# Kernel optimization log

Hardware: AMD Instinct MI355X
Metric: run time of the kernel (lower is better)

## Reference

```python
import jax, jax.numpy as jnp
import numpy as np

B, T, D = 2, 2048, 1024
H, DH = 16, 64          # num_heads, size_per_head
NU = H * DH             # num_units == 1024


def setup_inputs() -> dict:
    key = jax.random.key(0)
    ks = jax.random.split(key, 8)
    s = 0.02
    return {
        "queries": jax.random.normal(ks[0], (B, T, D), jnp.float32),
        "keys": jax.random.normal(ks[1], (B, T, D), jnp.float32),
        "Wq": jax.random.normal(ks[2], (D, NU), jnp.float32) * s,
        "bq": jnp.zeros((NU,), jnp.float32),
        "Wk": jax.random.normal(ks[3], (D, NU), jnp.float32) * s,
        "bk": jnp.zeros((NU,), jnp.float32),
        "Wv": jax.random.normal(ks[4], (D, NU), jnp.float32) * s,
        "bv": jnp.zeros((NU,), jnp.float32),
    }


def reference(queries, keys, Wq, bq, Wk, bk, Wv, bv):
    # QKV projections
    q = queries @ Wq + bq            # [B, T, NU]
    k = keys @ Wk + bk
    v = keys @ Wv + bv
    # split heads: [B, T, H, DH] -> [B, H, T, DH]
    q_ = q.reshape(B, T, H, DH).transpose(0, 2, 1, 3)
    k_ = k.reshape(B, T, H, DH).transpose(0, 2, 1, 3)
    v_ = v.reshape(B, T, H, DH).transpose(0, 2, 1, 3)
    # scores scaled by num_units**-0.5 (full hidden dim, as in source)
    scores = jnp.einsum("bhqd,bhkd->bhqk", q_, k_) * (NU ** -0.5)
    # causal mask: triu(ones).T == lower-triangular; zeros -> -inf
    causal = jnp.tril(jnp.ones((T, T), bool))
    scores = jnp.where(causal, scores, -jnp.inf)
    weights = jax.nn.softmax(scores, axis=-1)   # [B, H, T, T]
    # dropout is identity in eval/reference
    out = jnp.einsum("bhqk,bhkd->bhqd", weights, v_)  # [B, H, T, DH]
    # merge heads back to [B, T, NU]
    out = out.transpose(0, 2, 1, 3).reshape(B, T, NU)
    return out, weights
```

## Files before the change

kernel.cpp:

```cpp
#include <hip/hip_runtime.h>
#include <cstddef>
#include <cstdint>

namespace {
constexpr int B_ = 2, T_ = 2048, D_ = 1024, H_ = 16, DH_ = 64, NU_ = 1024;
constexpr float SCALE = 0.03125f;
constexpr size_t OUT_ELEMS = (size_t)B_ * T_ * NU_;
}

using f4  = __attribute__((ext_vector_type(4))) float;
using s8v = __attribute__((ext_vector_type(8))) short;
using s4v = __attribute__((ext_vector_type(4))) short;

#define MFMA16(a, b, c) __builtin_amdgcn_mfma_f32_16x16x32_bf16((a), (b), (c), 0, 0, 0)

__device__ __forceinline__ float4 ld4(const float* p) { return *reinterpret_cast<const float4*>(p); }
__device__ __forceinline__ void st4(float* p, const float4 v) { *reinterpret_cast<float4*>(p) = v; }
__device__ __forceinline__ short f2bf(float f) {
    union { float f; uint32_t u; } v{f};
    uint32_t r = (v.u + 0x7fffu + ((v.u >> 16) & 1u)) >> 16;
    return (short)r;
}

#if __has_builtin(__builtin_amdgcn_global_load_lds)
#define HAVE_GLOAD_LDS 1
__device__ __forceinline__ void load_lds16(const void* g, void* l) {
    __builtin_amdgcn_global_load_lds(
        (const __attribute__((address_space(1))) void*)g,
        (__attribute__((address_space(3))) void*)l, 16, 0, 0);
}
#else
#define HAVE_GLOAD_LDS 0
#endif

__global__ __launch_bounds__(256) void cvt_x_kernel(
    const float* __restrict__ q, const float* __restrict__ k,
    short* __restrict__ qx, short* __restrict__ kx)
{
    const float* src = blockIdx.y ? k : q;
    short* dst       = blockIdx.y ? kx : qx;
    size_t i = ((size_t)blockIdx.x * 256 + threadIdx.x) * 8;
    float4 a = ld4(src + i), b = ld4(src + i + 4);
    s8v o = { f2bf(a.x), f2bf(a.y), f2bf(a.z), f2bf(a.w),
              f2bf(b.x), f2bf(b.y), f2bf(b.z), f2bf(b.w) };
    *reinterpret_cast<s8v*>(dst + i) = o;
}

__global__ __launch_bounds__(256) void cvt_w_kernel(
    const float* __restrict__ Wq, const float* __restrict__ Wk,
    const float* __restrict__ Wv, short* __restrict__ wt3)
{
    const int z = blockIdx.z;
    const float* W = (z == 0) ? Wq : (z == 1) ? Wk : Wv;
    short* dst = wt3 + (size_t)z * D_ * NU_;
    const int n0 = blockIdx.x * 64, k0 = blockIdx.y * 64;
    __shared__ float tl[64][68];
    const int rr = threadIdx.x >> 2, cc = (threadIdx.x & 3) * 16;
    const float* s = W + (size_t)(k0 + rr) * NU_ + n0 + cc;
    st4(&tl[rr][cc + 0],  ld4(s + 0));
    st4(&tl[rr][cc + 4],  ld4(s + 4));
    st4(&tl[rr][cc + 8],  ld4(s + 8));
    st4(&tl[rr][cc + 12], ld4(s + 12));
    __syncthreads();
    short* d = dst + (size_t)(n0 + rr) * D_ + k0 + cc;
#pragma unroll
    for (int c = 0; c < 4; ++c) {
        s4v o = { f2bf(tl[cc + c * 4 + 0][rr]), f2bf(tl[cc + c * 4 + 1][rr]),
                  f2bf(tl[cc + c * 4 + 2][rr]), f2bf(tl[cc + c * 4 + 3][rr]) };
        *reinterpret_cast<s4v*>(d + c * 4) = o;
    }
}

__global__ __launch_bounds__(256) void proj_mfma(
    const short* __restrict__ qx, const short* __restrict__ kx,
    const short* __restrict__ wt3,
    const float* __restrict__ bq, const float* __restrict__ bk,
    const float* __restrict__ bv,
    short* __restrict__ qb, short* __restrict__ kb, short* __restrict__ vt)
{
    const int lin = blockIdx.z * 256 + blockIdx.y * 8 + blockIdx.x;
    const int virt = (lin & 7) * 96 + (lin >> 3);
    const int z = virt >> 8, rem = virt & 255;
    const int m0 = (rem >> 3) * 128, n0 = (rem & 7) * 128;

    const short* __restrict__ X  = (z == 0) ? qx : kx;
    const short* __restrict__ Wt = wt3 + (size_t)z * D_ * NU_;
    const float* __restrict__ bias = (z == 0) ? bq : (z == 1) ? bk : bv;

    const int t = threadIdx.x, w = t >> 6, l = t & 63;
    const int lr = l & 15, lg = l >> 4;
    const int wr = w >> 1, wc = w & 1;

    __shared__ short Asl[128 * 64];
    __shared__ short Bsl[128 * 64];

    f4 acc[4][4];
#pragma unroll
    for (int m = 0; m < 4; ++m)
#pragma unroll
        for (int n = 0; n < 4; ++n) acc[m][n] = (f4){0.f, 0.f, 0.f, 0.f};

    for (int k0 = 0; k0 < D_; k0 += 64) {
#if HAVE_GLOAD_LDS
#pragma unroll
        for (int j = 0; j < 4; ++j) {
            const int c0 = (w * 4 + j) * 64;
            const int c  = c0 + l;
            const int row = c >> 3, qo = (c & 7) * 8;
            load_lds16(X  + (size_t)(m0 + row) * D_ + k0 + qo, (char*)Asl + (size_t)c0 * 16);
            load_lds16(Wt + (size_t)(n0 + row) * D_ + k0 + qo, (char*)Bsl + (size_t)c0 * 16);
        }
        __syncthreads();
#else
        {
            const int sr = t >> 1, sc = (t & 1) * 32;
            s8v a0 = *reinterpret_cast<const s8v*>(X  + (size_t)(m0 + sr) * D_ + k0 + sc);
            s8v a1 = *reinterpret_cast<const s8v*>(X  + (size_t)(m0 + sr) * D_ + k0 + sc + 8);
            s8v a2 = *reinterpret_cast<const s8v*>(X  + (size_t)(m0 + sr) * D_ + k0 + sc + 16);
            s8v a3 = *reinterpret_cast<const s8v*>(X  + (size_t)(m0 + sr) * D_ + k0 + sc + 24);
            s8v b0 = *reinterpret_cast<const s8v*>(Wt + (size_t)(n0 + sr) * D_ + k0 + sc);
            s8v b1 = *reinterpret_cast<const s8v*>(Wt + (size_t)(n0 + sr) * D_ + k0 + sc + 8);
            s8v b2 = *reinterpret_cast<const s8v*>(Wt + (size_t)(n0 + sr) * D_ + k0 + sc + 16);
            s8v b3 = *reinterpret_cast<const s8v*>(Wt + (size_t)(n0 + sr) * D_ + k0 + sc + 24);
            __syncthreads();
            *reinterpret_cast<s8v*>(&Asl[sr * 64 + sc])      = a0;
            *reinterpret_cast<s8v*>(&Asl[sr * 64 + sc + 8])  = a1;
            *reinterpret_cast<s8v*>(&Asl[sr * 64 + sc + 16]) = a2;
            *reinterpret_cast<s8v*>(&Asl[sr * 64 + sc + 24]) = a3;
            *reinterpret_cast<s8v*>(&Bsl[sr * 64 + sc])      = b0;
            *reinterpret_cast<s8v*>(&Bsl[sr * 64 + sc + 8])  = b1;
            *reinterpret_cast<s8v*>(&Bsl[sr * 64 + sc + 16]) = b2;
            *reinterpret_cast<s8v*>(&Bsl[sr * 64 + sc + 24]) = b3;
            __syncthreads();
        }
#endif

#pragma unroll
        for (int kk = 0; kk < 2; ++kk) {
            s8v af[4], bf[4];
#pragma unroll
            for (int m = 0; m < 4; ++m)
                af[m] = *reinterpret_cast<const s8v*>(
                    &Asl[(wr * 64 + m * 16 + lr) * 64 + kk * 32 + lg * 8]);
#pragma unroll
            for (int n = 0; n < 4; ++n)
                bf[n] = *reinterpret_cast<const s8v*>(
                    &Bsl[(wc * 64 + n * 16 + lr) * 64 + kk * 32 + lg * 8]);
#pragma unroll
            for (int m = 0; m < 4; ++m)
#pragma unroll
                for (int n = 0; n < 4; ++n)
                    acc[m][n] = MFMA16(af[m], bf[n], acc[m][n]);
        }
        __syncthreads();
    }

    if (z < 2) {
        short* __restrict__ Y = (z == 0) ? qb : kb;
#pragma unroll
        for (int n = 0; n < 4; ++n) {
            const int col = n0 + wc * 64 + n * 16 + lr;
            const float bval = bias[col];
#pragma unroll
            for (int m = 0; m < 4; ++m) {
                const int row0 = m0 + wr * 64 + m * 16 + lg * 4;
#pragma unroll
                for (int r = 0; r < 4; ++r)
                    Y[(size_t)(row0 + r) * NU_ + col] = f2bf(acc[m][n][r] + bval);
            }
        }
    } else {
#pragma unroll
        for (int n = 0; n < 4; ++n) {
            const int col = n0 + wc * 64 + n * 16 + lr;
            const float bval = bias[col];
            const int hh = col >> 6, dd = col & 63;
#pragma unroll
            for (int m = 0; m < 4; ++m) {
                const int Mi = m0 + wr * 64 + m * 16 + lg * 4;
                const int bb = Mi >> 11, t0 = Mi & 2047;
                s4v o = { f2bf(acc[m][n][0] + bval), f2bf(acc[m][n][1] + bval),
                          f2bf(acc[m][n][2] + bval), f2bf(acc[m][n][3] + bval) };
                *reinterpret_cast<s4v*>(vt + ((size_t)(bb * 16 + hh) * 64 + dd) * T_ + t0) = o;
            }
        }
    }
}

__global__ __launch_bounds__(256) void attn_pv_mfma(
    const short* __restrict__ qb, const short* __restrict__ kb,
    const short* __restrict__ vt, float* __restrict__ rsws,
    float* __restrict__ out)
{
    const int lin = blockIdx.x;
    const int xcd = lin & 7, v = lin >> 3;
    const int bh  = xcd * 4 + (v >> 5);
    const int g64 = 31 - (v & 31);
    const int b = bh >> 4, h = bh & 15;
    const int r0 = g64 * 64;
    const int t = threadIdx.x, w = t >> 6, l = t & 63;
    const int lr = l & 15, lg = l >> 4;
    const int tile16 = g64;

    __shared__ __align__(16) char smem[32 * 1024 + 1024];
    short* Pl    = (short*)smem;
    float* OA    = (float*)smem;
    float* rsbuf = (float*)(smem + 32 * 1024);

    const short* qrow0 = qb + (size_t)(b * T_ + r0 + lr) * NU_ + h * DH_ + lg * 8;
    s8v qf[4][2];
#pragma unroll
    for (int d = 0; d < 4; ++d) {
        qf[d][0] = *reinterpret_cast<const s8v*>(qrow0 + (size_t)d * 16 * NU_);
        qf[d][1] = *reinterpret_cast<const s8v*>(qrow0 + (size_t)d * 16 * NU_ + 32);
    }

    f4 acc[4][4];
#pragma unroll
    for (int d = 0; d < 4; ++d)
#pragma unroll
        for (int nt = 0; nt < 4; ++nt) acc[d][nt] = (f4){0.f, 0.f, 0.f, 0.f};
    float rsum[4] = {0.f, 0.f, 0.f, 0.f};
    const f4 zf = (f4){0.f, 0.f, 0.f, 0.f};
    const int sw = (lr & 7) << 3;
    const short* kbase0 = kb + (size_t)(b * T_) * NU_ + h * DH_ + lg * 8;
    short* PlW[4];
#pragma unroll
    for (int d = 0; d < 4; ++d) PlW[d] = &Pl[d * 4096 + w * 1024 + lr * 64];

    for (int ch = w; ch <= tile16; ch += 4) {
        const int jc = ch * 64;
        const bool diag = (ch == tile16);
        const short* kbase = kbase0 + (size_t)jc * NU_;

#pragma unroll
        for (int nt = 0; nt < 4; ++nt) {
            const short* kr = kbase + (size_t)(nt * 16 + lr) * NU_;
            s8v kf0 = *reinterpret_cast<const s8v*>(kr);
            s8v kf1 = *reinterpret_cast<const s8v*>(kr + 32);
            const int jl = nt * 16 + lg * 4;
#pragma unroll
            for (int d = 0; d < 4; ++d) {
                f4 a = MFMA16(kf0, qf[d][0], zf);
                f4 s = MFMA16(kf1, qf[d][1], a);
                float e[4];
#pragma unroll
                for (int r = 0; r < 4; ++r) {
                    float vv = __expf(s[r] * SCALE);
                    if (diag && (jl + r > d * 16 + lr)) vv = 0.f;
                    e[r] = vv;
                }
                rsum[d] += (e[0] + e[1]) + (e[2] + e[3]);
                s4v pv = { f2bf(e[0]), f2bf(e[1]), f2bf(e[2]), f2bf(e[3]) };
                *reinterpret_cast<s4v*>(PlW[d] + (jl ^ sw)) = pv;
            }
        }

        s8v pf[4][2];
#pragma unroll
        for (int d = 0; d < 4; ++d) {
            pf[d][0] = *reinterpret_cast<const s8v*>(PlW[d] + ((lg * 8) ^ sw));
            pf[d][1] = *reinterpret_cast<const s8v*>(PlW[d] + ((32 + lg * 8) ^ sw));
        }
#pragma unroll
        for (int nt = 0; nt < 4; ++nt) {
            const short* vr = vt + (size_t)(bh * 64 + nt * 16 + lr) * T_ + jc + lg * 8;
            s8v vf0 = *reinterpret_cast<const s8v*>(vr);
            s8v vf1 = *reinterpret_cast<const s8v*>(vr + 32);
#pragma unroll
            for (int d = 0; d < 4; ++d) {
                acc[d][nt] = MFMA16(pf[d][0], vf0, acc[d][nt]);
                acc[d][nt] = MFMA16(pf[d][1], vf1, acc[d][nt]);
            }
        }
    }

#pragma unroll
    for (int d = 0; d < 4; ++d) {
        rsum[d] += __shfl_xor(rsum[d], 16);
        rsum[d] += __shfl_xor(rsum[d], 32);
    }

    __syncthreads();
    if (lg == 0) {
#pragma unroll
        for (int d = 0; d < 4; ++d) rsbuf[d * 64 + w * 16 + lr] = rsum[d];
    }

#pragma unroll
    for (int d = 0; d < 4; ++d) {
#pragma unroll
        for (int nt = 0; nt < 4; ++nt)
            st4(&OA[(size_t)(w * 64 + l) * 16 + nt * 4], *(const float4*)&acc[d][nt]);
        __syncthreads();
        float osum[4] = {0.f, 0.f, 0.f, 0.f};
#pragma unroll
        for (int wv = 0; wv < 4; ++wv) {
            float4 p = *(const float4*)&OA[(size_t)(wv * 64 + l) * 16 + w * 4];
#pragma unroll
            for (int r = 0; r < 4; ++r) osum[r] += (&p.x)[r];
        }
#pragma unroll
        for (int r = 0; r < 4; ++r) {
            const int ro = lg * 4 + r;
            const float rt = rsbuf[d * 64 + ro] + rsbuf[d * 64 + 16 + ro]
                           + rsbuf[d * 64 + 32 + ro] + rsbuf[d * 64 + 48 + ro];
            out[(size_t)(b * T_ + r0 + d * 16 + ro) * NU_ + h * DH_ + w * 16 + lr] =
                osum[r] / rt;
        }
        if (w == 0 && t < 16)
            rsws[(size_t)bh * T_ + r0 + d * 16 + t] =
                rsbuf[d * 64 + t] + rsbuf[d * 64 + 16 + t]
                + rsbuf[d * 64 + 32 + t] + rsbuf[d * 64 + 48 + t];
        __syncthreads();
    }
}

__global__ __launch_bounds__(256) void attn_wts_mfma(
    const short* __restrict__ qb, const short* __restrict__ kb,
    const float* __restrict__ rsws, float* __restrict__ wts)
{
    const int lin = blockIdx.x;
    const int xcd = lin & 7, v = lin >> 3;
    const int bh  = xcd * 4 + (v >> 7);
    const int rem = v & 127;
    const int qt2 = 15 - (rem >> 3);
    const int jb  = rem & 7;
    const int b = bh >> 4, h = bh & 15;
    const int r0 = qt2 * 128;
    const int chmax = 2 * qt2 + 1;
    const int t = threadIdx.x, w = t >> 6, l = t & 63;
    const int lr = l & 15, lg = l >> 4;

    const int iA = r0 + w * 16 + lr;
    const int iB = iA + 64;

    const short* qrowA = qb + (size_t)(b * T_ + iA) * NU_ + h * DH_ + lg * 8;
    const s8v qA0 = *reinterpret_cast<const s8v*>(qrowA);
    const s8v qA1 = *reinterpret_cast<const s8v*>(qrowA + 32);
    const s8v qB0 = *reinterpret_cast<const s8v*>(qrowA + 64 * NU_);
    const s8v qB1 = *reinterpret_cast<const s8v*>(qrowA + 64 * NU_ + 32);
    const f4 zf = (f4){0.f, 0.f, 0.f, 0.f};

    const float invA = 1.f / rsws[(size_t)bh * T_ + iA];
    const float invB = 1.f / rsws[(size_t)bh * T_ + iB];
    float* const wrowA = &wts[((size_t)bh * T_ + iA) * T_];
    float* const wrowB = &wts[((size_t)bh * T_ + iB) * T_];
    const short* kbase0 = kb + (size_t)(b * T_) * NU_ + h * DH_ + lg * 8;

#pragma unroll
    for (int cx = 0; cx < 4; ++cx) {
        const int ch = jb * 4 + cx;
        const int jc = ch * 64;
        if (ch <= chmax) {
            const short* kbase = kbase0 + (size_t)jc * NU_;
            f4 sA[4], sB[4];
#pragma unroll
            for (int nt = 0; nt < 4; ++nt) {
                const short* kr = kbase + (size_t)(nt * 16 + lr) * NU_;
                s8v kf0 = *reinterpret_cast<const s8v*>(kr);
                s8v kf1 = *reinterpret_cast<const s8v*>(kr + 32);
                f4 aA = MFMA16(kf0, qA0, zf);
                sA[nt] = MFMA16(kf1, qA1, aA);
                f4 aB = MFMA16(kf0, qB0, zf);
                sB[nt] = MFMA16(kf1, qB1, aB);
            }
#pragma unroll
            for (int nt = 0; nt < 4; ++nt) {
                float4 oA, oB;
                float* eA = &oA.x;
                float* eB = &oB.x;
#pragma unroll
                for (int r = 0; r < 4; ++r) {
                    const int j = jc + nt * 16 + lg * 4 + r;
                    eA[r] = (j <= iA) ? __expf(sA[nt][r] * SCALE) * invA : 0.f;
                    eB[r] = (j <= iB) ? __expf(sB[nt][r] * SCALE) * invB : 0.f;
                }
                st4(wrowA + jc + nt * 16 + lg * 4, oA);
                st4(wrowB + jc + nt * 16 + lg * 4, oB);
            }
        } else {
            const float4 z4 = make_float4(0.f, 0.f, 0.f, 0.f);
#pragma unroll
            for (int half = 0; half < 2; ++half) {
                float* dst = &wts[((size_t)bh * T_ + r0 + half * 64 + (t >> 2)) * T_
                                  + jc + (t & 3) * 16];
                st4(dst + 0, z4); st4(dst + 4, z4);
                st4(dst + 8, z4); st4(dst + 12, z4);
            }
        }
    }
}

extern "C" void kernel_launch(void* const* d_in, const int* in_sizes, int n_in,
                              void* d_out, int out_size, void* d_ws, size_t ws_size,
                              hipStream_t stream)
{
    const float* queries = (const float*)d_in[0];
    const float* keys    = (const float*)d_in[1];
    const float* Wq = (const float*)d_in[2];
    const float* bq = (const float*)d_in[3];
    const float* Wk = (const float*)d_in[4];
    const float* bk = (const float*)d_in[5];
    const float* Wv = (const float*)d_in[6];
    const float* bv = (const float*)d_in[7];

    float* out = (float*)d_out;
    float* wts = out + OUT_ELEMS;

    short* qx = (short*)d_ws;
    short* kx = qx + (size_t)B_ * T_ * D_;
    short* wt = kx + (size_t)B_ * T_ * D_;
    short* qb = wt + (size_t)3 * D_ * NU_;
    short* kb = qb + (size_t)B_ * T_ * NU_;
    short* vt = kb + (size_t)B_ * T_ * NU_;
    float* rsws = (float*)(vt + (size_t)B_ * T_ * NU_);

    cvt_x_kernel<<<dim3((B_ * T_ * D_) / 2048, 2), 256, 0, stream>>>(queries, keys, qx, kx);
    cvt_w_kernel<<<dim3(16, 16, 3), 256, 0, stream>>>(Wq, Wk, Wv, wt);
    proj_mfma<<<dim3(8, 32, 3), 256, 0, stream>>>(
        qx, kx, wt, bq, bk, bv, qb, kb, vt);
    attn_pv_mfma<<<dim3(1024), 256, 0, stream>>>(qb, kb, vt, rsws, out);
    attn_wts_mfma<<<dim3(4096), 256, 0, stream>>>(qb, kb, rsws, wts);
}
```

Baseline: 283.8 us.

## Merge conversion kernels into one launch and add MFMA priority hints

The activation and weight bf16 conversion kernels become a single launch, with the block index picking which path runs. This removes one kernel launch and the gap between the two. In the attention kernels, the MFMA groups are wrapped in s_setprio raise/lower, and the score MFMAs are grouped ahead of the exp work so waves issuing matrix ops get scheduling priority. The merged kernel now allocates shared memory for blocks that never use it, and the priority hints may or may not improve interleaving.

```diff
diff --git a/kernel.cpp b/kernel.cpp
--- a/kernel.cpp
+++ b/kernel.cpp
@@ -33,28 +33,29 @@
 #define HAVE_GLOAD_LDS 0
 #endif
 
-__global__ __launch_bounds__(256) void cvt_x_kernel(
+__global__ __launch_bounds__(256) void cvt_all_kernel(
     const float* __restrict__ q, const float* __restrict__ k,
-    short* __restrict__ qx, short* __restrict__ kx)
+    const float* __restrict__ Wq, const float* __restrict__ Wk,
+    const float* __restrict__ Wv,
+    short* __restrict__ qx, short* __restrict__ kx, short* __restrict__ wt3)
 {
-    const float* src = blockIdx.y ? k : q;
-    short* dst       = blockIdx.y ? kx : qx;
-    size_t i = ((size_t)blockIdx.x * 256 + threadIdx.x) * 8;
-    float4 a = ld4(src + i), b = ld4(src + i + 4);
-    s8v o = { f2bf(a.x), f2bf(a.y), f2bf(a.z), f2bf(a.w),
-              f2bf(b.x), f2bf(b.y), f2bf(b.z), f2bf(b.w) };
-    *reinterpret_cast<s8v*>(dst + i) = o;
-}
-
-__global__ __launch_bounds__(256) void cvt_w_kernel(
-    const float* __restrict__ Wq, const float* __restrict__ Wk,
-    const float* __restrict__ Wv, short* __restrict__ wt3)
-{
-    const int z = blockIdx.z;
+    __shared__ float tl[64][68];
+    const int bid = blockIdx.x;
+    if (bid < 4096) {
+        const float* src = (bid < 2048) ? q : k;
+        short* dst       = (bid < 2048) ? qx : kx;
+        size_t i = ((size_t)(bid & 2047) * 256 + threadIdx.x) * 8;
+        float4 a = ld4(src + i), b = ld4(src + i + 4);
+        s8v o = { f2bf(a.x), f2bf(a.y), f2bf(a.z), f2bf(a.w),
+                  f2bf(b.x), f2bf(b.y), f2bf(b.z), f2bf(b.w) };
+        *reinterpret_cast<s8v*>(dst + i) = o;
+        return;
+    }
+    const int wb = bid - 4096;
+    const int z = wb >> 8, rem = wb & 255;
     const float* W = (z == 0) ? Wq : (z == 1) ? Wk : Wv;
     short* dst = wt3 + (size_t)z * D_ * NU_;
-    const int n0 = blockIdx.x * 64, k0 = blockIdx.y * 64;
-    __shared__ float tl[64][68];
+    const int n0 = (rem & 15) * 64, k0 = (rem >> 4) * 64;
     const int rr = threadIdx.x >> 2, cc = (threadIdx.x & 3) * 16;
     const float* s = W + (size_t)(k0 + rr) * NU_ + n0 + cc;
     st4(&tl[rr][cc + 0],  ld4(s + 0));
@@ -239,14 +240,20 @@
             s8v kf0 = *reinterpret_cast<const s8v*>(kr);
             s8v kf1 = *reinterpret_cast<const s8v*>(kr + 32);
             const int jl = nt * 16 + lg * 4;
+            f4 sD[4];
+            __builtin_amdgcn_s_setprio(1);
 #pragma unroll
             for (int d = 0; d < 4; ++d) {
                 f4 a = MFMA16(kf0, qf[d][0], zf);
-                f4 s = MFMA16(kf1, qf[d][1], a);
+                sD[d] = MFMA16(kf1, qf[d][1], a);
+            }
+            __builtin_amdgcn_s_setprio(0);
+#pragma unroll
+            for (int d = 0; d < 4; ++d) {
                 float e[4];
 #pragma unroll
                 for (int r = 0; r < 4; ++r) {
-                    float vv = __expf(s[r] * SCALE);
+                    float vv = __expf(sD[d][r] * SCALE);
                     if (diag && (jl + r > d * 16 + lr)) vv = 0.f;
                     e[r] = vv;
                 }
@@ -267,11 +274,13 @@
             const short* vr = vt + (size_t)(bh * 64 + nt * 16 + lr) * T_ + jc + lg * 8;
             s8v vf0 = *reinterpret_cast<const s8v*>(vr);
             s8v vf1 = *reinterpret_cast<const s8v*>(vr + 32);
+            __builtin_amdgcn_s_setprio(1);
 #pragma unroll
             for (int d = 0; d < 4; ++d) {
                 acc[d][nt] = MFMA16(pf[d][0], vf0, acc[d][nt]);
                 acc[d][nt] = MFMA16(pf[d][1], vf1, acc[d][nt]);
             }
+            __builtin_amdgcn_s_setprio(0);
         }
     }
 
@@ -360,10 +369,12 @@
                 const short* kr = kbase + (size_t)(nt * 16 + lr) * NU_;
                 s8v kf0 = *reinterpret_cast<const s8v*>(kr);
                 s8v kf1 = *reinterpret_cast<const s8v*>(kr + 32);
+                __builtin_amdgcn_s_setprio(1);
                 f4 aA = MFMA16(kf0, qA0, zf);
                 sA[nt] = MFMA16(kf1, qA1, aA);
                 f4 aB = MFMA16(kf0, qB0, zf);
                 sB[nt] = MFMA16(kf1, qB1, aB);
+                __builtin_amdgcn_s_setprio(0);
             }
 #pragma unroll
             for (int nt = 0; nt < 4; ++nt) {
@@ -416,8 +427,8 @@
     short* vt = kb + (size_t)B_ * T_ * NU_;
     float* rsws = (float*)(vt + (size_t)B_ * T_ * NU_);
 
-    cvt_x_kernel<<<dim3((B_ * T_ * D_) / 2048, 2), 256, 0, stream>>>(queries, keys, qx, kx);
-    cvt_w_kernel<<<dim3(16, 16, 3), 256, 0, stream>>>(Wq, Wk, Wv, wt);
+    cvt_all_kernel<<<dim3(4864), 256, 0, stream>>>(
+        queries, keys, Wq, Wk, Wv, qx, kx, wt);
     proj_mfma<<<dim3(8, 32, 3), 256, 0, stream>>>(
         qx, kx, wt, bq, bk, bv, qb, kb, vt);
     attn_pv_mfma<<<dim3(1024), 256, 0, stream>>>(qb, kb, vt, rsws, out);
```

Result: no change. 287.3 us (+1.2%).
